# Optimization experiments

Hardware: AMD Instinct MI355X
Metric: run time of the kernel (lower is better)

The kernel has to match this reference:

```python
import jax, jax.numpy as jnp
import numpy as np

B, S, L, H, D, DF = 2, 1024, 2, 8, 512, 2048
DK = D // H  # head dim (dk == dv == 64)
EPS = 1e-5


def _ln(x, g, b):
    m = jnp.mean(x, axis=-1, keepdims=True)
    v = jnp.mean((x - m) ** 2, axis=-1, keepdims=True)
    return (x - m) / jnp.sqrt(v + EPS) * g + b


def setup_inputs() -> dict:
    key = jax.random.key(0)
    ks = jax.random.split(key, 8)
    sd = 1.0 / np.sqrt(D)
    sf = 1.0 / np.sqrt(DF)
    inp = {
        "src": jax.random.normal(ks[0], (B, S, D), jnp.float32),
        "Wq": jax.random.normal(ks[1], (L, D, D), jnp.float32) * sd,
        "bq": jnp.zeros((L, D), jnp.float32),
        "Wk": jax.random.normal(ks[2], (L, D, D), jnp.float32) * sd,
        "bk": jnp.zeros((L, D), jnp.float32),
        "Wv": jax.random.normal(ks[3], (L, D, D), jnp.float32) * sd,
        "bv": jnp.zeros((L, D), jnp.float32),
        "Wo": jax.random.normal(ks[4], (L, D, D), jnp.float32) * sd,
        "bo": jnp.zeros((L, D), jnp.float32),
        "W1": jax.random.normal(ks[5], (L, D, DF), jnp.float32) * sd,
        "b1": jnp.zeros((L, DF), jnp.float32),
        "W2": jax.random.normal(ks[6], (L, DF, D), jnp.float32) * sf,
        "b2": jnp.zeros((L, D), jnp.float32),
        "g1": jnp.ones((L, D), jnp.float32),
        "be1": jnp.zeros((L, D), jnp.float32),
        "g2": jnp.ones((L, D), jnp.float32),
        "be2": jnp.zeros((L, D), jnp.float32),
        "gf": jnp.ones((D,), jnp.float32),
        "bef": jnp.zeros((D,), jnp.float32),
    }
    return inp


def _heads(x):
    # [B,S,D] -> [B,H,S,DK]
    return x.reshape(B, S, H, DK).transpose(0, 2, 1, 3)


def _causal_linear_attention(q, k, v):
    # Faithful to torch: cumsum of per-step KV outer products, then query contraction.
    kv = jnp.einsum("bhsk,bhsv->bhskv", k, v)      # [B,H,S,DK,DK]
    cum = jnp.cumsum(kv, axis=2)                     # prefix sums over sequence
    return jnp.einsum("bhsk,bhskv->bhsv", q, cum)   # [B,H,S,DK]


def reference(src, Wq, bq, Wk, bk, Wv, bv, Wo, bo, W1, b1, W2, b2,
              g1, be1, g2, be2, gf, bef):
    x = src
    for i in range(L):
        q = _heads(x @ Wq[i] + bq[i])
        k = _heads(x @ Wk[i] + bk[i])
        v = _heads(x @ Wv[i] + bv[i])
        att = _causal_linear_attention(q, k, v)
        att = att.transpose(0, 2, 1, 3).reshape(B, S, D)
        att = att @ Wo[i] + bo[i]
        x = _ln(x + att, g1[i], be1[i])              # post-norm (normalize_before=False)
        ff = jax.nn.relu(x @ W1[i] + b1[i]) @ W2[i] + b2[i]
        x = _ln(x + ff, g2[i], be2[i])
    return _ln(x, gf, bef)                            # final encoder LayerNorm
```

## Files before the change

### kernel.cpp

```cpp
#include <hip/hip_runtime.h>
#include <hip/hip_bf16.h>

#define DEV static __device__ __forceinline__

typedef __attribute__((ext_vector_type(8))) short short8;
typedef __attribute__((ext_vector_type(4))) float f32x4;

DEV unsigned short f2b(float f){
  unsigned int u = __float_as_uint(f);
  return (unsigned short)((u + 0x7FFFu + ((u >> 16) & 1u)) >> 16);
}
DEV float b2f(unsigned short h){ return __uint_as_float(((unsigned int)h) << 16); }
DEV float load_in(const void* p, size_t i, int isbf){
  return isbf ? b2f(((const unsigned short*)p)[i]) : ((const float*)p)[i];
}
DEV void load_lds16(const unsigned short* g, unsigned short* l){
  __builtin_amdgcn_global_load_lds(
      (const __attribute__((address_space(1))) void*)g,
      (__attribute__((address_space(3))) void*)l, 16, 0, 0);
}

DEV int detect_isbf_block(const void* src){
  __shared__ int cnt[4];
  int tid = threadIdx.x;
  float v = b2f(((const unsigned short*)src)[2 * tid]);
  float av = fabsf(v);
  bool sane = ((av < 64.0f) && (av > 9.5e-7f)) || (v == 0.0f);
  unsigned long long m = __ballot(sane);
  if ((tid & 63) == 0) cnt[tid >> 6] = __popcll(m);
  __syncthreads();
  int tot = cnt[0] + cnt[1] + cnt[2] + cnt[3];
  __syncthreads();
  return tot > 128;
}

struct WDesc { const void* src; long src_off; unsigned short* dst; int K; int N; int tstart; };
struct SDesc { const void* src; int src_off; int dstart; };
struct IngestParams {
  WDesc w[12];
  SDesc s[22];
  float* sdst; int stotal;
  const void* src;
  unsigned short* xb;
};

__global__ __launch_bounds__(256) void ingest_all(IngestParams P){
  __shared__ float tile[32][33];
  int b = blockIdx.x, tid = threadIdx.x;
  int isbf = detect_isbf_block(P.src);
  if (b < 6144){
    int t = 0;
    #pragma unroll
    for (int i = 1; i < 12; ++i) if (b >= P.w[i].tstart) t = i;
    WDesc d = P.w[t];
    int r = b - d.tstart;
    int tiles_x = d.N >> 5;
    int tx = r % tiles_x, ty = r / tiles_x;
    int lx = tid & 31, ly = tid >> 5;
    #pragma unroll
    for (int i = 0; i < 4; ++i){
      int row = ty*32 + ly + i*8;
      int col = tx*32 + lx;
      tile[ly + i*8][lx] = load_in(d.src, (size_t)d.src_off + (size_t)row*d.N + col, isbf);
    }
    __syncthreads();
    #pragma unroll
    for (int i = 0; i < 4; ++i){
      int orow = tx*32 + ly + i*8;
      int ocol = ty*32 + lx;
      d.dst[(size_t)orow*d.K + ocol] = f2b(tile[lx][ly + i*8]);
    }
    return;
  }
  int mb = b - 6144;
  if (mb < 4096){
    int i = mb*256 + tid;
    P.xb[i] = f2b(load_in(P.src, (size_t)i, isbf));
  } else {
    int i = (mb - 4096)*256 + tid;
    if (i < P.stotal){
      int t = 0;
      #pragma unroll
      for (int j = 1; j < 22; ++j) if (i >= P.s[j].dstart) t = j;
      P.sdst[i] = load_in(P.s[t].src, (size_t)P.s[t].src_off + (i - P.s[t].dstart), isbf);
    }
  }
}

struct GemmArgs {
  const unsigned short* A;
  const unsigned short* Bt;
  const float* bias;
  float* Cf;
  unsigned short* Cb;
  int K;
  int lda, ldb, ldc;
  int cshift, cmask;
  size_t cstride;
  size_t cfz;
  int relu;
};

template<int BM>
__global__ __launch_bounds__(256) void gemm_bt(GemmArgs g){
  constexpr int NI = BM / 64;
  constexpr int NJ = 4;
  constexpr int APASS = BM / 32;
  constexpr int WROWS = BM / 4;
  __shared__ __align__(16) unsigned short sA[2][BM*64];
  __shared__ __align__(16) unsigned short sB[2][64*64];
  int tid = threadIdx.x;
  int koff = blockIdx.z * g.K;
  int K = g.K, lda = g.lda, ldb = g.ldb;
  size_t bm = (size_t)blockIdx.y * BM, bn = (size_t)blockIdx.x * 64;
  int lane = tid & 63, wv = tid >> 6, quad = lane >> 4, l16 = lane & 15;
  int wm = wv * WROWS;
  f32x4 acc[NI][NJ];
  #pragma unroll
  for (int i=0;i<NI;++i)
    #pragma unroll
    for (int j=0;j<NJ;++j) acc[i][j] = (f32x4){0.f,0.f,0.f,0.f};
  int srow = tid >> 3;
  int schunk = (tid & 7) ^ (srow & 7);
  const unsigned short* Ap = g.A  + (bm + srow)*lda + koff + schunk*8;
  const unsigned short* Bp = g.Bt + (bn + srow)*ldb + koff + schunk*8;

  #define STAGE(buf, ko)                                                      \
    do {                                                                      \
      _Pragma("unroll")                                                       \
      for (int p = 0; p < APASS; ++p)                                         \
        load_lds16(Ap + (size_t)(p*32)*lda + (ko), &sA[buf][p*2048 + tid*8]); \
      _Pragma("unroll")                                                       \
      for (int p = 0; p < 2; ++p)                                             \
        load_lds16(Bp + (size_t)(p*32)*ldb + (ko), &sB[buf][p*2048 + tid*8]); \
    } while (0)

  STAGE(0, 0);
  asm volatile("s_waitcnt vmcnt(0)" ::: "memory");
  __builtin_amdgcn_s_barrier();

  int nt = K >> 6;
  int cur = 0;
  for (int t = 0; t < nt; ++t){
    if (t + 1 < nt){
      STAGE(cur ^ 1, (t + 1) * 64);
      __builtin_amdgcn_sched_barrier(0);
    }
    #pragma unroll
    for (int kk = 0; kk < 2; ++kk){
      short8 af[NI], bfv[NJ];
      #pragma unroll
      for (int i=0;i<NI;++i){
        int row = wm + i*16 + l16;
        int ch  = (kk*4 + quad) ^ (row & 7);
        af[i] = *(const short8*)&sA[cur][row*64 + ch*8];
      }
      #pragma unroll
      for (int j=0;j<NJ;++j){
        int row = j*16 + l16;
        int ch  = (kk*4 + quad) ^ (row & 7);
        bfv[j] = *(const short8*)&sB[cur][row*64 + ch*8];
      }
      #pragma unroll
      for (int i=0;i<NI;++i)
        #pragma unroll
        for (int j=0;j<NJ;++j)
          acc[i][j] = __builtin_amdgcn_mfma_f32_16x16x32_bf16(af[i], bfv[j], acc[i][j], 0,0,0);
    }
    if (t + 1 < nt){
      asm volatile("s_waitcnt vmcnt(0)" ::: "memory");
      __builtin_amdgcn_s_barrier();
    }
    cur ^= 1;
  }
  #undef STAGE

  float* Cf = g.Cf ? g.Cf + (size_t)blockIdx.z * g.cfz : nullptr;
  unsigned short* Cb = g.Cb;
  #pragma unroll
  for (int j=0;j<NJ;++j){
    int col = (int)bn + j*16 + l16;
    float bv = g.bias ? g.bias[col] : 0.f;
    size_t cbase = ((size_t)(col >> g.cshift))*g.cstride + (col & g.cmask);
    #pragma unroll
    for (int i=0;i<NI;++i){
      #pragma unroll
      for (int r=0;r<4;++r){
        int row = (int)bm + wm + i*16 + quad*4 + r;
        float v = acc[i][j][r] + bv;
        if (g.relu) v = fmaxf(v, 0.f);
        size_t idx = cbase + (size_t)row*g.ldc;
        if (Cf) Cf[idx] = v;
        if (Cb) Cb[idx] = f2b(v);
      }
    }
  }
}

#define ATT_S 1024
#define ATT_D 512

__global__ __launch_bounds__(256) void attn_state_kernel(
    const unsigned short* k, const unsigned short* v, float* states)
{
  __shared__ __align__(16) unsigned short sVt[64*72];
  __shared__ __align__(16) unsigned short sKt[64*72];
  int tid = threadIdx.x;
  int c = blockIdx.x, bh = blockIdx.y;
  int b = bh >> 3, h = bh & 7;
  const size_t base = ((size_t)b*ATT_S + (size_t)c*64)*ATT_D + h*64;
  int lane = tid & 63, wv = tid >> 6, quad = lane >> 4, l16 = lane & 15;

  int t = lane, vc = wv*8;
  const unsigned short* vp = v + base + (size_t)t*ATT_D;
  const unsigned short* kp = k + base + (size_t)t*ATT_D;
  float4 v0 = *(const float4*)(vp + vc);
  float4 v1 = *(const float4*)(vp + vc + 32);
  float4 k0 = *(const float4*)(kp + vc);
  float4 k1 = *(const float4*)(kp + vc + 32);
  {
    const unsigned short* pv0 = (const unsigned short*)&v0;
    const unsigned short* pv1 = (const unsigned short*)&v1;
    const unsigned short* pk0 = (const unsigned short*)&k0;
    const unsigned short* pk1 = (const unsigned short*)&k1;
    #pragma unroll
    for (int e = 0; e < 8; ++e){
      sVt[(vc+e)*72 + t]    = pv0[e];
      sVt[(vc+32+e)*72 + t] = pv1[e];
      sKt[(vc+e)*72 + t]    = pk0[e];
      sKt[(vc+32+e)*72 + t] = pk1[e];
    }
  }
  __syncthreads();

  f32x4 acc[4];
  #pragma unroll
  for (int j=0;j<4;++j) acc[j] = (f32x4){0.f,0.f,0.f,0.f};
  #pragma unroll
  for (int kk=0;kk<2;++kk){
    short8 a = *(const short8*)&sVt[(wv*16 + l16)*72 + kk*32 + quad*8];
    #pragma unroll
    for (int j=0;j<4;++j){
      short8 bb = *(const short8*)&sKt[(j*16 + l16)*72 + kk*32 + quad*8];
      acc[j] = __builtin_amdgcn_mfma_f32_16x16x32_bf16(a, bb, acc[j], 0,0,0);
    }
  }
  float* st = states + ((size_t)bh*16 + c)*4096;
  #pragma unroll
  for (int j=0;j<4;++j)
    #pragma unroll
    for (int rr=0;rr<4;++rr)
      st[(wv*16 + quad*4 + rr)*64 + j*16 + l16] = acc[j][rr];
}

__global__ __launch_bounds__(256) void attn_out_kernel(
    const unsigned short* q, const unsigned short* k, const unsigned short* v,
    const float* states, unsigned short* att)
{
  __shared__ __align__(16) unsigned short sQ [64*72];
  __shared__ __align__(16) unsigned short sK [64*72];
  __shared__ __align__(16) unsigned short sVt[64*72];
  __shared__ __align__(16) float sKV[64*68];
  int tid = threadIdx.x;
  int c = blockIdx.x, bh = blockIdx.y;
  int b = bh >> 3, h = bh & 7;
  const size_t base = ((size_t)b*ATT_S + (size_t)c*64)*ATT_D + h*64;
  int lane = tid & 63, wv = tid >> 6, quad = lane >> 4, l16 = lane & 15;

  float4 racc[4];
  #pragma unroll
  for (int u=0;u<4;++u) racc[u] = (float4){0.f,0.f,0.f,0.f};
  const float* sbase = states + (size_t)bh*16*4096;
  for (int cc = 0; cc < c; ++cc){
    const float4* sp = (const float4*)(sbase + (size_t)cc*4096);
    #pragma unroll
    for (int u=0;u<4;++u){
      float4 t4 = sp[tid + u*256];
      racc[u].x += t4.x; racc[u].y += t4.y; racc[u].z += t4.z; racc[u].w += t4.w;
    }
  }
  #pragma unroll
  for (int u=0;u<4;++u){
    int e = (tid + u*256)*4;
    int row = e >> 6, col = e & 63;
    *(float4*)&sKV[row*68 + col] = racc[u];
  }

  int r = tid >> 2, c8 = (tid & 3)*8;
  const unsigned short* qp = q + base + (size_t)r*ATT_D;
  const unsigned short* kp = k + base + (size_t)r*ATT_D;
  float4 q0 = *(const float4*)(qp + c8);
  float4 q1 = *(const float4*)(qp + c8 + 32);
  float4 k0 = *(const float4*)(kp + c8);
  float4 k1 = *(const float4*)(kp + c8 + 32);
  int t = lane, vc = wv*8;
  const unsigned short* vp = v + base + (size_t)t*ATT_D;
  float4 v0 = *(const float4*)(vp + vc);
  float4 v1 = *(const float4*)(vp + vc + 32);
  *(float4*)&sQ[r*72 + c8]      = q0;
  *(float4*)&sQ[r*72 + c8 + 32] = q1;
  *(float4*)&sK[r*72 + c8]      = k0;
  *(float4*)&sK[r*72 + c8 + 32] = k1;
  {
    const unsigned short* pv0 = (const unsigned short*)&v0;
    const unsigned short* pv1 = (const unsigned short*)&v1;
    #pragma unroll
    for (int e=0;e<8;++e){
      sVt[(vc+e)*72 + t]    = pv0[e];
      sVt[(vc+32+e)*72 + t] = pv1[e];
    }
  }
  __syncthreads();

  f32x4 accS[4];
  #pragma unroll
  for (int j=0;j<4;++j) accS[j] = (f32x4){0.f,0.f,0.f,0.f};
  #pragma unroll
  for (int kk=0;kk<2;++kk){
    short8 a = *(const short8*)&sQ[(wv*16 + l16)*72 + kk*32 + quad*8];
    #pragma unroll
    for (int j=0;j<4;++j){
      short8 bb = *(const short8*)&sK[(j*16 + l16)*72 + kk*32 + quad*8];
      accS[j] = __builtin_amdgcn_mfma_f32_16x16x32_bf16(a, bb, accS[j], 0,0,0);
    }
  }
  __syncthreads();

  #pragma unroll
  for (int j=0;j<4;++j)
    #pragma unroll
    for (int rr=0;rr<4;++rr){
      int i  = wv*16 + quad*4 + rr;
      int cj = j*16 + l16;
      sK[i*72 + cj] = f2b((i >= cj) ? accS[j][rr] : 0.f);
    }

  f32x4 accO[4];
  #pragma unroll
  for (int j=0;j<4;++j) accO[j] = (f32x4){0.f,0.f,0.f,0.f};
  #pragma unroll
  for (int kk=0;kk<2;++kk){
    short8 a = *(const short8*)&sQ[(wv*16 + l16)*72 + kk*32 + quad*8];
    #pragma unroll
    for (int j=0;j<4;++j){
      const float* pf = &sKV[(j*16 + l16)*68 + kk*32 + quad*8];
      short8 bb;
      #pragma unroll
      for (int e=0;e<8;++e) ((unsigned short*)&bb)[e] = f2b(pf[e]);
      accO[j] = __builtin_amdgcn_mfma_f32_16x16x32_bf16(a, bb, accO[j], 0,0,0);
    }
  }
  __syncthreads();

  #pragma unroll
  for (int kk=0;kk<2;++kk){
    short8 a = *(const short8*)&sK[(wv*16 + l16)*72 + kk*32 + quad*8];
    #pragma unroll
    for (int j=0;j<4;++j){
      short8 bb = *(const short8*)&sVt[(j*16 + l16)*72 + kk*32 + quad*8];
      accO[j] = __builtin_amdgcn_mfma_f32_16x16x32_bf16(a, bb, accO[j], 0,0,0);
    }
  }
  #pragma unroll
  for (int j=0;j<4;++j)
    #pragma unroll
    for (int rr=0;rr<4;++rr){
      int i  = wv*16 + quad*4 + rr;
      int cj = j*16 + l16;
      att[base + (size_t)i*ATT_D + cj] = f2b(accO[j][rr]);
    }
}

__global__ __launch_bounds__(256) void add_ln_kernel(
    const float* x, const void* xalt, const float* p, int np, const float* bias,
    const float* g, const float* bta, const float* g2, const float* b2,
    float* outf, unsigned short* outb, void* outd, const void* dsrc, int rows)
{
  int isbf = 0;
  if (dsrc) isbf = detect_isbf_block(dsrc);
  int row = blockIdx.x*4 + (threadIdx.x >> 6);
  int lane = threadIdx.x & 63;
  if (row >= rows) return;
  float a[8];
  if (xalt){
    if (isbf){
      const unsigned short* xr = (const unsigned short*)xalt + (size_t)row*512;
      const unsigned short* p0 = xr + lane*4;
      const unsigned short* p1 = xr + 256 + lane*4;
      #pragma unroll
      for (int e=0;e<4;++e){ a[e] = b2f(p0[e]); a[4+e] = b2f(p1[e]); }
    } else {
      const float* xr = (const float*)xalt + (size_t)row*512;
      *(float4*)&a[0] = *(const float4*)(xr + lane*4);
      *(float4*)&a[4] = *(const float4*)(xr + 256 + lane*4);
    }
  } else {
    const float* xr = x + (size_t)row*512;
    *(float4*)&a[0] = *(const float4*)(xr + lane*4);
    *(float4*)&a[4] = *(const float4*)(xr + 256 + lane*4);
  }
  for (int s = 0; s < np; ++s){
    const float* pr = p + (size_t)s*1048576 + (size_t)row*512;
    float yb[8];
    *(float4*)&yb[0] = *(const float4*)(pr + lane*4);
    *(float4*)&yb[4] = *(const float4*)(pr + 256 + lane*4);
    #pragma unroll
    for (int e=0;e<8;++e) a[e] += yb[e];
  }
  if (bias){
    float bb2[8];
    *(float4*)&bb2[0] = *(const float4*)(bias + lane*4);
    *(float4*)&bb2[4] = *(const float4*)(bias + 256 + lane*4);
    #pragma unroll
    for (int e=0;e<8;++e) a[e] += bb2[e];
  }
  float s = 0.f, qq = 0.f;
  #pragma unroll
  for (int e=0;e<8;++e){ s += a[e]; qq += a[e]*a[e]; }
  #pragma unroll
  for (int off=32; off>0; off>>=1){
    s  += __shfl_xor(s,  off, 64);
    qq += __shfl_xor(qq, off, 64);
  }
  float mean = s * (1.f/512.f);
  float var  = qq * (1.f/512.f) - mean*mean;
  float rstd = rsqrtf(var + 1e-5f);
  float gg[8], bb[8];
  *(float4*)&gg[0] = *(const float4*)(g + lane*4);
  *(float4*)&gg[4] = *(const float4*)(g + 256 + lane*4);
  *(float4*)&bb[0] = *(const float4*)(bta + lane*4);
  *(float4*)&bb[4] = *(const float4*)(bta + 256 + lane*4);
  #pragma unroll
  for (int e=0;e<8;++e) a[e] = (a[e]-mean)*rstd*gg[e] + bb[e];
  if (g2){
    float s2 = 0.f, q2 = 0.f;
    #pragma unroll
    for (int e=0;e<8;++e){ s2 += a[e]; q2 += a[e]*a[e]; }
    #pragma unroll
    for (int off=32; off>0; off>>=1){
      s2 += __shfl_xor(s2, off, 64);
      q2 += __shfl_xor(q2, off, 64);
    }
    float m2 = s2 * (1.f/512.f);
    float v2 = q2 * (1.f/512.f) - m2*m2;
    float r2 = rsqrtf(v2 + 1e-5f);
    float gg2[8], bb22[8];
    *(float4*)&gg2[0]  = *(const float4*)(g2 + lane*4);
    *(float4*)&gg2[4]  = *(const float4*)(g2 + 256 + lane*4);
    *(float4*)&bb22[0] = *(const float4*)(b2 + lane*4);
    *(float4*)&bb22[4] = *(const float4*)(b2 + 256 + lane*4);
    #pragma unroll
    for (int e=0;e<8;++e) a[e] = (a[e]-m2)*r2*gg2[e] + bb22[e];
  }
  if (outf){
    float* orow = outf + (size_t)row*512;
    *(float4*)(orow + lane*4)       = *(float4*)&a[0];
    *(float4*)(orow + 256 + lane*4) = *(float4*)&a[4];
  }
  if (outb){
    unsigned short* orow = outb + (size_t)row*512;
    #pragma unroll
    for (int e=0;e<4;++e){ orow[lane*4+e] = f2b(a[e]); orow[256+lane*4+e] = f2b(a[4+e]); }
  }
  if (outd){
    if (isbf){
      unsigned short* od = (unsigned short*)outd + (size_t)row*512;
      #pragma unroll
      for (int e=0;e<4;++e){ od[lane*4+e] = f2b(a[e]); od[256+lane*4+e] = f2b(a[4+e]); }
    } else {
      float* od = (float*)outd + (size_t)row*512;
      *(float4*)(od + lane*4)       = *(float4*)&a[0];
      *(float4*)(od + 256 + lane*4) = *(float4*)&a[4];
    }
  }
}

extern "C" void kernel_launch(void* const* d_in, const int* in_sizes, int n_in,
                              void* d_out, int out_size, void* d_ws, size_t ws_size,
                              hipStream_t stream)
{
  (void)in_sizes; (void)n_in; (void)out_size; (void)ws_size;
  const void* src = d_in[0];
  const void* Wq = d_in[1];  const void* bq = d_in[2];
  const void* Wk = d_in[3];  const void* bk = d_in[4];
  const void* Wv = d_in[5];  const void* bv = d_in[6];
  const void* Wo = d_in[7];  const void* bo = d_in[8];
  const void* W1 = d_in[9];  const void* b1 = d_in[10];
  const void* W2 = d_in[11]; const void* b2 = d_in[12];
  const void* g1 = d_in[13]; const void* be1 = d_in[14];
  const void* g2 = d_in[15]; const void* be2 = d_in[16];
  const void* gf = d_in[17]; const void* bef = d_in[18];

  char* W = (char*)d_ws;
  float* smalls          = (float*)(W + 256);
  unsigned short* wt     = (unsigned short*)(W + 65536);
  float* x_f             = (float*)(W + 12648448);
  unsigned short* x_b    = (unsigned short*)(W + 16842752);
  unsigned short* q_b    = (unsigned short*)(W + 18939904);
  unsigned short* att_b  = (unsigned short*)(W + 25231360);
  float* pp              = (float*)(W + 27328512);
  unsigned short* h1_b   = (unsigned short*)(W + 44105728);
  float* states          = (float*)(W + 44105728);
  unsigned short* k_b = q_b + 1048576;
  unsigned short* v_b = q_b + 2097152;

  IngestParams ip;
  {
    const void* wsrc[6] = {Wq, Wk, Wv, Wo, W1, W2};
    int wK[6] = {512,512,512,512,512,2048};
    int wN[6] = {512,512,512,512,2048,512};
    long wsz[6] = {262144,262144,262144,262144,1048576,1048576};
    int tstart = 0; size_t dsto = 0;
    for (int l=0;l<2;++l)
      for (int ti=0;ti<6;++ti){
        int idx = l*6+ti;
        ip.w[idx].src = wsrc[ti];
        ip.w[idx].src_off = (long)l * wsz[ti];
        ip.w[idx].dst = wt + dsto;
        ip.w[idx].K = wK[ti]; ip.w[idx].N = wN[ti];
        ip.w[idx].tstart = tstart;
        tstart += (wK[ti]/32)*(wN[ti]/32);
        dsto += (size_t)wsz[ti];
      }
    const void* ss[10] = {bq,bk,bv,bo,b1,b2,g1,be1,g2,be2};
    int slen[10] = {512,512,512,512,2048,512,512,512,512,512};
    int dcur = 0, di = 0;
    for (int l=0;l<2;++l)
      for (int ti=0;ti<10;++ti){
        ip.s[di].src = ss[ti];
        ip.s[di].src_off = l * slen[ti];
        ip.s[di].dstart = dcur;
        dcur += slen[ti]; ++di;
      }
    ip.s[20].src = gf;  ip.s[20].src_off = 0; ip.s[20].dstart = dcur; dcur += 512;
    ip.s[21].src = bef; ip.s[21].src_off = 0; ip.s[21].dstart = dcur; dcur += 512;
    ip.sdst = smalls; ip.stotal = dcur;
    ip.src = src; ip.xb = x_b;
    ingest_all<<<dim3(10296), 256, 0, stream>>>(ip);
  }

  for (int l = 0; l < 2; ++l){
    unsigned short* WqkvT = wt + (size_t)l*3145728;
    unsigned short* WoT   = WqkvT + 786432;
    unsigned short* W1T   = WqkvT + 1048576;
    unsigned short* W2T   = WqkvT + 2097152;
    float* base  = smalls + l*6656;
    float* p_bqkv= base;
    float* p_bo  = base + 1536;
    float* p_b1  = base + 2048;
    float* p_b2  = base + 4096;
    float* p_g1  = base + 4608;
    float* p_be1 = base + 5120;
    float* p_g2  = base + 5632;
    float* p_be2 = base + 6144;

    GemmArgs qkv = {};
    qkv.A = x_b; qkv.Bt = WqkvT; qkv.bias = p_bqkv;
    qkv.Cf = nullptr; qkv.Cb = q_b;
    qkv.K = 512; qkv.lda = 512; qkv.ldb = 512; qkv.ldc = 512;
    qkv.cshift = 9; qkv.cmask = 511; qkv.cstride = 1048576; qkv.cfz = 0; qkv.relu = 0;
    gemm_bt<64><<<dim3(24,32,1), 256, 0, stream>>>(qkv);

    attn_state_kernel<<<dim3(16,16), 256, 0, stream>>>(k_b, v_b, states);
    attn_out_kernel<<<dim3(16,16), 256, 0, stream>>>(q_b, k_b, v_b, states, att_b);

    GemmArgs go = {};
    go.A = att_b; go.Bt = WoT; go.bias = nullptr;
    go.Cf = pp; go.Cb = nullptr;
    go.K = 256; go.lda = 512; go.ldb = 512; go.ldc = 512;
    go.cshift = 30; go.cmask = 0x3fffffff; go.cstride = 0; go.cfz = 1048576; go.relu = 0;
    gemm_bt<64><<<dim3(8,32,2), 256, 0, stream>>>(go);

    if (l == 0)
      add_ln_kernel<<<dim3(512), 256, 0, stream>>>(nullptr, src, pp, 2, p_bo,
                                                   p_g1, p_be1, nullptr, nullptr,
                                                   x_f, x_b, nullptr, src, 2048);
    else
      add_ln_kernel<<<dim3(512), 256, 0, stream>>>(x_f, nullptr, pp, 2, p_bo,
                                                   p_g1, p_be1, nullptr, nullptr,
                                                   x_f, x_b, nullptr, nullptr, 2048);

    GemmArgs f1 = {};
    f1.A = x_b; f1.Bt = W1T; f1.bias = p_b1;
    f1.Cf = nullptr; f1.Cb = h1_b;
    f1.K = 512; f1.lda = 512; f1.ldb = 512; f1.ldc = 2048;
    f1.cshift = 30; f1.cmask = 0x3fffffff; f1.cstride = 0; f1.cfz = 0; f1.relu = 1;
    gemm_bt<64><<<dim3(32,32,1), 256, 0, stream>>>(f1);

    GemmArgs f2 = {};
    f2.A = h1_b; f2.Bt = W2T; f2.bias = nullptr;
    f2.Cf = pp; f2.Cb = nullptr;
    f2.K = 512; f2.lda = 2048; f2.ldb = 2048; f2.ldc = 512;
    f2.cshift = 30; f2.cmask = 0x3fffffff; f2.cstride = 0; f2.cfz = 1048576; f2.relu = 0;
    gemm_bt<64><<<dim3(8,32,4), 256, 0, stream>>>(f2);

    if (l == 0){
      add_ln_kernel<<<dim3(512), 256, 0, stream>>>(x_f, nullptr, pp, 4, p_b2,
                                                   p_g2, p_be2, nullptr, nullptr,
                                                   x_f, x_b, nullptr, nullptr, 2048);
    } else {
      add_ln_kernel<<<dim3(512), 256, 0, stream>>>(x_f, nullptr, pp, 4, p_b2,
                                                   p_g2, p_be2,
                                                   smalls + 13312, smalls + 13824,
                                                   nullptr, nullptr, d_out, src, 2048);
    }
  }
}
```

Before: 246.8 us.

## Split attention chunks into half-blocks and halve FFN2 split-K

The attention state and output kernels now launch a z-dimension of 2. Each block handles 32 rows of a 64-row chunk, so twice as many blocks share the work. The state kernel writes per-half states that the output kernel then sums, which doubles its prefix-sum reads. Separately, the FFN down-projection drops from 4-way to 2-way split-K, and the following add-LayerNorm reads fewer partials. That reduces partial-buffer traffic but gives fewer blocks for that GEMM.

```diff
diff --git a/kernel.cpp b/kernel.cpp
--- a/kernel.cpp
+++ b/kernel.cpp
@@ -206,29 +206,23 @@
   __shared__ __align__(16) unsigned short sVt[64*72];
   __shared__ __align__(16) unsigned short sKt[64*72];
   int tid = threadIdx.x;
-  int c = blockIdx.x, bh = blockIdx.y;
+  int c = blockIdx.x, bh = blockIdx.y, z = blockIdx.z;
   int b = bh >> 3, h = bh & 7;
   const size_t base = ((size_t)b*ATT_S + (size_t)c*64)*ATT_D + h*64;
   int lane = tid & 63, wv = tid >> 6, quad = lane >> 4, l16 = lane & 15;
 
-  int t = lane, vc = wv*8;
-  const unsigned short* vp = v + base + (size_t)t*ATT_D;
-  const unsigned short* kp = k + base + (size_t)t*ATT_D;
-  float4 v0 = *(const float4*)(vp + vc);
-  float4 v1 = *(const float4*)(vp + vc + 32);
-  float4 k0 = *(const float4*)(kp + vc);
-  float4 k1 = *(const float4*)(kp + vc + 32);
+  int t = tid & 31, cb = (tid >> 5) * 8;
+  const unsigned short* vp = v + base + (size_t)(z*32 + t)*ATT_D + cb;
+  const unsigned short* kp = k + base + (size_t)(z*32 + t)*ATT_D + cb;
+  float4 v0 = *(const float4*)vp;
+  float4 k0 = *(const float4*)kp;
   {
     const unsigned short* pv0 = (const unsigned short*)&v0;
-    const unsigned short* pv1 = (const unsigned short*)&v1;
     const unsigned short* pk0 = (const unsigned short*)&k0;
-    const unsigned short* pk1 = (const unsigned short*)&k1;
     #pragma unroll
     for (int e = 0; e < 8; ++e){
-      sVt[(vc+e)*72 + t]    = pv0[e];
-      sVt[(vc+32+e)*72 + t] = pv1[e];
-      sKt[(vc+e)*72 + t]    = pk0[e];
-      sKt[(vc+32+e)*72 + t] = pk1[e];
+      sVt[(cb+e)*72 + t] = pv0[e];
+      sKt[(cb+e)*72 + t] = pk0[e];
     }
   }
   __syncthreads();
@@ -236,16 +230,13 @@
   f32x4 acc[4];
   #pragma unroll
   for (int j=0;j<4;++j) acc[j] = (f32x4){0.f,0.f,0.f,0.f};
-  #pragma unroll
-  for (int kk=0;kk<2;++kk){
-    short8 a = *(const short8*)&sVt[(wv*16 + l16)*72 + kk*32 + quad*8];
-    #pragma unroll
-    for (int j=0;j<4;++j){
-      short8 bb = *(const short8*)&sKt[(j*16 + l16)*72 + kk*32 + quad*8];
-      acc[j] = __builtin_amdgcn_mfma_f32_16x16x32_bf16(a, bb, acc[j], 0,0,0);
-    }
-  }
-  float* st = states + ((size_t)bh*16 + c)*4096;
+  short8 a = *(const short8*)&sVt[(wv*16 + l16)*72 + quad*8];
+  #pragma unroll
+  for (int j=0;j<4;++j){
+    short8 bb = *(const short8*)&sKt[(j*16 + l16)*72 + quad*8];
+    acc[j] = __builtin_amdgcn_mfma_f32_16x16x32_bf16(a, bb, acc[j], 0,0,0);
+  }
+  float* st = states + (((size_t)bh*16 + c)*2 + z)*4096;
   #pragma unroll
   for (int j=0;j<4;++j)
     #pragma unroll
@@ -257,21 +248,24 @@
     const unsigned short* q, const unsigned short* k, const unsigned short* v,
     const float* states, unsigned short* att)
 {
-  __shared__ __align__(16) unsigned short sQ [64*72];
+  __shared__ __align__(16) unsigned short sQ [32*72];
   __shared__ __align__(16) unsigned short sK [64*72];
   __shared__ __align__(16) unsigned short sVt[64*72];
   __shared__ __align__(16) float sKV[64*68];
   int tid = threadIdx.x;
-  int c = blockIdx.x, bh = blockIdx.y;
+  int c = blockIdx.x, bh = blockIdx.y, z = blockIdx.z;
+  int half = z*32;
   int b = bh >> 3, h = bh & 7;
   const size_t base = ((size_t)b*ATT_S + (size_t)c*64)*ATT_D + h*64;
   int lane = tid & 63, wv = tid >> 6, quad = lane >> 4, l16 = lane & 15;
+  int rowg = (wv & 1) * 16;
+  int cp   = (wv >> 1) * 2;
 
   float4 racc[4];
   #pragma unroll
   for (int u=0;u<4;++u) racc[u] = (float4){0.f,0.f,0.f,0.f};
-  const float* sbase = states + (size_t)bh*16*4096;
-  for (int cc = 0; cc < c; ++cc){
+  const float* sbase = states + (size_t)bh*32*4096;
+  for (int cc = 0; cc < 2*c; ++cc){
     const float4* sp = (const float4*)(sbase + (size_t)cc*4096);
     #pragma unroll
     for (int u=0;u<4;++u){
@@ -286,22 +280,25 @@
     *(float4*)&sKV[row*68 + col] = racc[u];
   }
 
-  int r = tid >> 2, c8 = (tid & 3)*8;
-  const unsigned short* qp = q + base + (size_t)r*ATT_D;
-  const unsigned short* kp = k + base + (size_t)r*ATT_D;
-  float4 q0 = *(const float4*)(qp + c8);
-  float4 q1 = *(const float4*)(qp + c8 + 32);
-  float4 k0 = *(const float4*)(kp + c8);
-  float4 k1 = *(const float4*)(kp + c8 + 32);
-  int t = lane, vc = wv*8;
-  const unsigned short* vp = v + base + (size_t)t*ATT_D;
-  float4 v0 = *(const float4*)(vp + vc);
-  float4 v1 = *(const float4*)(vp + vc + 32);
-  *(float4*)&sQ[r*72 + c8]      = q0;
-  *(float4*)&sQ[r*72 + c8 + 32] = q1;
-  *(float4*)&sK[r*72 + c8]      = k0;
-  *(float4*)&sK[r*72 + c8 + 32] = k1;
   {
+    int r = tid >> 3, c8 = (tid & 7) * 8;
+    const unsigned short* qp = q + base + (size_t)(half + r)*ATT_D + c8;
+    float4 q0 = *(const float4*)qp;
+    *(float4*)&sQ[r*72 + c8] = q0;
+  }
+  {
+    int r = tid >> 2, c8 = (tid & 3) * 8;
+    const unsigned short* kp = k + base + (size_t)r*ATT_D;
+    float4 k0 = *(const float4*)(kp + c8);
+    float4 k1 = *(const float4*)(kp + c8 + 32);
+    *(float4*)&sK[r*72 + c8]      = k0;
+    *(float4*)&sK[r*72 + c8 + 32] = k1;
+  }
+  {
+    int t = lane, vc = wv*8;
+    const unsigned short* vp = v + base + (size_t)t*ATT_D;
+    float4 v0 = *(const float4*)(vp + vc);
+    float4 v1 = *(const float4*)(vp + vc + 32);
     const unsigned short* pv0 = (const unsigned short*)&v0;
     const unsigned short* pv1 = (const unsigned short*)&v1;
     #pragma unroll
@@ -312,38 +309,38 @@
   }
   __syncthreads();
 
-  f32x4 accS[4];
-  #pragma unroll
-  for (int j=0;j<4;++j) accS[j] = (f32x4){0.f,0.f,0.f,0.f};
+  f32x4 accS[2];
+  #pragma unroll
+  for (int j=0;j<2;++j) accS[j] = (f32x4){0.f,0.f,0.f,0.f};
   #pragma unroll
   for (int kk=0;kk<2;++kk){
-    short8 a = *(const short8*)&sQ[(wv*16 + l16)*72 + kk*32 + quad*8];
-    #pragma unroll
-    for (int j=0;j<4;++j){
-      short8 bb = *(const short8*)&sK[(j*16 + l16)*72 + kk*32 + quad*8];
+    short8 a = *(const short8*)&sQ[(rowg + l16)*72 + kk*32 + quad*8];
+    #pragma unroll
+    for (int j=0;j<2;++j){
+      short8 bb = *(const short8*)&sK[((cp+j)*16 + l16)*72 + kk*32 + quad*8];
       accS[j] = __builtin_amdgcn_mfma_f32_16x16x32_bf16(a, bb, accS[j], 0,0,0);
     }
   }
   __syncthreads();
 
   #pragma unroll
-  for (int j=0;j<4;++j)
+  for (int j=0;j<2;++j)
     #pragma unroll
     for (int rr=0;rr<4;++rr){
-      int i  = wv*16 + quad*4 + rr;
-      int cj = j*16 + l16;
-      sK[i*72 + cj] = f2b((i >= cj) ? accS[j][rr] : 0.f);
-    }
-
-  f32x4 accO[4];
-  #pragma unroll
-  for (int j=0;j<4;++j) accO[j] = (f32x4){0.f,0.f,0.f,0.f};
+      int il = rowg + quad*4 + rr;
+      int cj = (cp+j)*16 + l16;
+      sK[il*72 + cj] = f2b(((half + il) >= cj) ? accS[j][rr] : 0.f);
+    }
+
+  f32x4 accO[2];
+  #pragma unroll
+  for (int j=0;j<2;++j) accO[j] = (f32x4){0.f,0.f,0.f,0.f};
   #pragma unroll
   for (int kk=0;kk<2;++kk){
-    short8 a = *(const short8*)&sQ[(wv*16 + l16)*72 + kk*32 + quad*8];
-    #pragma unroll
-    for (int j=0;j<4;++j){
-      const float* pf = &sKV[(j*16 + l16)*68 + kk*32 + quad*8];
+    short8 a = *(const short8*)&sQ[(rowg + l16)*72 + kk*32 + quad*8];
+    #pragma unroll
+    for (int j=0;j<2;++j){
+      const float* pf = &sKV[((cp+j)*16 + l16)*68 + kk*32 + quad*8];
       short8 bb;
       #pragma unroll
       for (int e=0;e<8;++e) ((unsigned short*)&bb)[e] = f2b(pf[e]);
@@ -354,19 +351,19 @@
 
   #pragma unroll
   for (int kk=0;kk<2;++kk){
-    short8 a = *(const short8*)&sK[(wv*16 + l16)*72 + kk*32 + quad*8];
-    #pragma unroll
-    for (int j=0;j<4;++j){
-      short8 bb = *(const short8*)&sVt[(j*16 + l16)*72 + kk*32 + quad*8];
+    short8 a = *(const short8*)&sK[(rowg + l16)*72 + kk*32 + quad*8];
+    #pragma unroll
+    for (int j=0;j<2;++j){
+      short8 bb = *(const short8*)&sVt[((cp+j)*16 + l16)*72 + kk*32 + quad*8];
       accO[j] = __builtin_amdgcn_mfma_f32_16x16x32_bf16(a, bb, accO[j], 0,0,0);
     }
   }
   #pragma unroll
-  for (int j=0;j<4;++j)
+  for (int j=0;j<2;++j)
     #pragma unroll
     for (int rr=0;rr<4;++rr){
-      int i  = wv*16 + quad*4 + rr;
-      int cj = j*16 + l16;
+      int i  = half + rowg + quad*4 + rr;
+      int cj = (cp+j)*16 + l16;
       att[base + (size_t)i*ATT_D + cj] = f2b(accO[j][rr]);
     }
 }
@@ -561,8 +558,8 @@
     qkv.cshift = 9; qkv.cmask = 511; qkv.cstride = 1048576; qkv.cfz = 0; qkv.relu = 0;
     gemm_bt<64><<<dim3(24,32,1), 256, 0, stream>>>(qkv);
 
-    attn_state_kernel<<<dim3(16,16), 256, 0, stream>>>(k_b, v_b, states);
-    attn_out_kernel<<<dim3(16,16), 256, 0, stream>>>(q_b, k_b, v_b, states, att_b);
+    attn_state_kernel<<<dim3(16,16,2), 256, 0, stream>>>(k_b, v_b, states);
+    attn_out_kernel<<<dim3(16,16,2), 256, 0, stream>>>(q_b, k_b, v_b, states, att_b);
 
     GemmArgs go = {};
     go.A = att_b; go.Bt = WoT; go.bias = nullptr;
@@ -590,16 +587,16 @@
     GemmArgs f2 = {};
     f2.A = h1_b; f2.Bt = W2T; f2.bias = nullptr;
     f2.Cf = pp; f2.Cb = nullptr;
-    f2.K = 512; f2.lda = 2048; f2.ldb = 2048; f2.ldc = 512;
+    f2.K = 1024; f2.lda = 2048; f2.ldb = 2048; f2.ldc = 512;
     f2.cshift = 30; f2.cmask = 0x3fffffff; f2.cstride = 0; f2.cfz = 1048576; f2.relu = 0;
-    gemm_bt<64><<<dim3(8,32,4), 256, 0, stream>>>(f2);
+    gemm_bt<64><<<dim3(8,32,2), 256, 0, stream>>>(f2);
 
     if (l == 0){
-      add_ln_kernel<<<dim3(512), 256, 0, stream>>>(x_f, nullptr, pp, 4, p_b2,
+      add_ln_kernel<<<dim3(512), 256, 0, stream>>>(x_f, nullptr, pp, 2, p_b2,
                                                    p_g2, p_be2, nullptr, nullptr,
                                                    x_f, x_b, nullptr, nullptr, 2048);
     } else {
-      add_ln_kernel<<<dim3(512), 256, 0, stream>>>(x_f, nullptr, pp, 4, p_b2,
+      add_ln_kernel<<<dim3(512), 256, 0, stream>>>(x_f, nullptr, pp, 2, p_b2,
                                                    p_g2, p_be2,
                                                    smalls + 13312, smalls + 13824,
                                                    nullptr, nullptr, d_out, src, 2048);
```

Measured after the change: 259.9 us. +5.3%, slower.
